# Performance work log

Measured on AMD Instinct MI355X. Metric: run time of the kernel, lower is better.

The kernel has to match this reference:

```python
import jax, jax.numpy as jnp
import numpy as np

NUM_ENT = 10000
NUM_REL = 230
S_DIM = 96
T_DIM = 32
DIM = S_DIM + T_DIM  # 128
N = 32768   # neighbors
Q = 4096    # unique query entities
E = 32768   # pooling edges
B = 1024    # batch triples
BN_EPS = 1e-5


def setup_inputs() -> dict:
    key = jax.random.key(0)
    ks = jax.random.split(key, 32)
    inp = {}
    inp["neighbor_idx"] = jax.random.randint(ks[0], (N,), 0, NUM_ENT)
    inp["rel_id"] = jax.random.randint(ks[1], (N,), 0, 2 * NUM_REL)
    inp["years"] = jax.random.uniform(ks[2], (N, 1), jnp.float32)
    inp["months"] = jax.random.uniform(ks[3], (N, 1), jnp.float32)
    inp["days"] = jax.random.uniform(ks[4], (N, 1), jnp.float32)
    inp["pool_src"] = jax.random.randint(ks[5], (E,), 0, N)
    inp["pool_dst"] = jax.random.randint(ks[6], (E,), 0, Q)
    inp["head_pos"] = jax.random.randint(ks[7], (B,), 0, Q)
    inp["tail_pos"] = jax.random.randint(ks[8], (B,), 0, Q)
    inp["rels"] = jax.random.randint(ks[9], (B,), 0, NUM_REL)
    # parameters (xavier-ish scales)
    inp["ent_embs"] = jax.random.normal(ks[10], (NUM_ENT, S_DIM), jnp.float32) * 0.05
    names = ["y_freq", "y_phi", "y_amp", "m_freq", "m_phi", "m_amp", "d_freq", "d_phi", "d_amp"]
    for i, n in enumerate(names):
        inp[n] = jax.random.normal(ks[11 + i], (NUM_ENT, T_DIM), jnp.float32) * 0.05
    inp["rel_embs"] = jax.random.normal(ks[20], (NUM_REL, DIM), jnp.float32) * 0.05
    inp["W"] = jax.random.normal(ks[21], (2 * NUM_REL, DIM, DIM), jnp.float32) * (1.0 / np.sqrt(DIM))
    inp["b"] = jnp.zeros((2 * NUM_REL, DIM), jnp.float32)
    inp["gamma"] = jnp.ones((2 * NUM_REL, DIM), jnp.float32)
    inp["beta"] = jnp.zeros((2 * NUM_REL, DIM), jnp.float32)
    return inp


def _forward(ent_embs, y_freq, y_phi, y_amp, m_freq, m_phi, m_amp,
             d_freq, d_phi, d_amp, rel_embs, W, b, gamma, beta,
             years, months, days,
             neighbor_idx, rel_id, pool_src, pool_dst, head_pos, tail_pos, rels):
    # diachronic time embedding: amp * sin(freq * t + phi), summed over y/m/d
    ty = y_amp[neighbor_idx] * jnp.sin(y_freq[neighbor_idx] * years + y_phi[neighbor_idx])
    tm = m_amp[neighbor_idx] * jnp.sin(m_freq[neighbor_idx] * months + m_phi[neighbor_idx])
    td = d_amp[neighbor_idx] * jnp.sin(d_freq[neighbor_idx] * days + d_phi[neighbor_idx])
    x = jnp.concatenate([ent_embs[neighbor_idx], ty + tm + td], axis=1)  # [N, DIM]

    # per-relation Linear (gather weights per neighbor)
    z = jnp.einsum('nd,nde->ne', x, W[rel_id]) + b[rel_id]  # [N, DIM]

    # per-relation-bucket BatchNorm (training stats, biased var); skipped for singleton buckets
    R2 = 2 * NUM_REL
    cnt = jax.ops.segment_sum(jnp.ones((z.shape[0],), z.dtype), rel_id, num_segments=R2)
    denom = jnp.maximum(cnt, 1.0)[:, None]
    mean = jax.ops.segment_sum(z, rel_id, num_segments=R2) / denom
    var = jax.ops.segment_sum(z * z, rel_id, num_segments=R2) / denom - mean * mean
    var = jnp.maximum(var, 0.0)
    zn = (z - mean[rel_id]) * jax.lax.rsqrt(var[rel_id] + BN_EPS) * gamma[rel_id] + beta[rel_id]
    z = jnp.where((cnt[rel_id] > 1.0)[:, None], zn, z)
    z = jax.nn.relu(z)

    # average pooling of neighbor features per query entity (PoolingLayer 'avg')
    psum = jax.ops.segment_sum(z[pool_src], pool_dst, num_segments=Q)
    pcnt = jax.ops.segment_sum(jnp.ones((pool_src.shape[0],), z.dtype), pool_dst, num_segments=Q)
    emb = psum / jnp.maximum(pcnt, 1.0)[:, None]  # [Q, DIM]

    # TransE-style scoring: -||h + r - t||_2 (dropout p=0 / eval mode)
    diff = emb[head_pos] + rel_embs[rels] - emb[tail_pos]
    return -jnp.sqrt(jnp.sum(diff * diff, axis=1))


def reference(neighbor_idx, rel_id, years, months, days, pool_src, pool_dst,
              head_pos, tail_pos, rels, ent_embs, y_freq, y_phi, y_amp,
              m_freq, m_phi, m_amp, d_freq, d_phi, d_amp, rel_embs, W, b, gamma, beta):
    return _forward(ent_embs, y_freq, y_phi, y_amp, m_freq, m_phi, m_amp,
                    d_freq, d_phi, d_amp, rel_embs, W, b, gamma, beta,
                    years, months, days,
                    neighbor_idx, rel_id, pool_src, pool_dst, head_pos, tail_pos, rels)
```

## Files before the change

kernel.cpp:

```cpp
#include <hip/hip_runtime.h>
#include <math.h>

#define NUM_ENT 10000
#define NUM_REL 230
#define R2      460
#define S_DIM   96
#define T_DIM   32
#define DIM     128
#define N_NBR   32768
#define Q_ENT   4096
#define E_EDGE  32768
#define B_TRI   1024
#define BN_EPS  1e-5f
#define CHUNK   64

typedef __attribute__((ext_vector_type(8))) short bf16x8;
typedef __attribute__((ext_vector_type(4))) float f32x4;

__device__ __forceinline__ unsigned short f2bf(float f) {
    unsigned int u = __float_as_uint(f);
    u = (u + 0x7FFFu + ((u >> 16) & 1u)) >> 16;
    return (unsigned short)u;
}

__device__ __forceinline__ int XIDX(int m, int d) {
    return (m * DIM + d) ^ ((m & 7) << 3);
}

__global__ void k_zero(int* __restrict__ p, int n4) {
    int i = blockIdx.x * blockDim.x + threadIdx.x;
    if (i < n4) ((int4*)p)[i] = make_int4(0, 0, 0, 0);
}

__global__ __launch_bounds__(256, 2) void k_front(
    const float* __restrict__ W, unsigned short* __restrict__ Wfrag,
    const int* __restrict__ rel, const int* __restrict__ pdst,
    int* __restrict__ hist_rel, int* __restrict__ hist_dst)
{
    const int t = threadIdx.x;
    if (blockIdx.x >= R2) {
        const int i = (blockIdx.x - R2) * 256 + t;
        if (i < N_NBR) atomicAdd(&hist_rel[rel[i]], 1);
        if (i < E_EDGE) atomicAdd(&hist_dst[pdst[i]], 1);
        return;
    }
    const int r = blockIdx.x;
    __shared__ float Wl[DIM * DIM];
    {
        const float4* Wg = (const float4*)(W + (size_t)r * DIM * DIM);
        float4* Wl4 = (float4*)Wl;
        #pragma unroll
        for (int i = 0; i < 16; ++i)
            Wl4[t + i * 256] = Wg[t + i * 256];
    }
    __syncthreads();
    unsigned short* dst = Wfrag + (size_t)r * DIM * DIM;
    #pragma unroll
    for (int it = 0; it < 8; ++it) {
        const int id = t + it * 256;
        const int lane = id & 63;
        const int h    = (id >> 6) & 1;
        const int wv   = (id >> 7) & 3;
        const int kk   = (id >> 9) & 3;
        const int n  = 32 * wv + 16 * h + (lane & 15);
        const int kb = 32 * kk + 8 * (lane >> 4);
        ushort4 lo, hi;
        lo.x = f2bf(Wl[(kb + 0) * DIM + n]);
        lo.y = f2bf(Wl[(kb + 1) * DIM + n]);
        lo.z = f2bf(Wl[(kb + 2) * DIM + n]);
        lo.w = f2bf(Wl[(kb + 3) * DIM + n]);
        hi.x = f2bf(Wl[(kb + 4) * DIM + n]);
        hi.y = f2bf(Wl[(kb + 5) * DIM + n]);
        hi.z = f2bf(Wl[(kb + 6) * DIM + n]);
        hi.w = f2bf(Wl[(kb + 7) * DIM + n]);
        *(ushort4*)&dst[id * 8]     = lo;
        *(ushort4*)&dst[id * 8 + 4] = hi;
    }
}

__global__ void k_scan_both(const int* __restrict__ hist_rel, int* __restrict__ offsets,
                            int* __restrict__ cur_rel,
                            const int* __restrict__ hist_dst, int* __restrict__ dst_off,
                            int* __restrict__ cur_dst)
{
    __shared__ int s[1024];
    const int t = threadIdx.x;
    if (blockIdx.x == 0) {
        const int h = (t < R2) ? hist_rel[t] : 0;
        if (t < 512) s[t] = h;
        __syncthreads();
        for (int off = 1; off < 512; off <<= 1) {
            int a = (t >= off && t < 512) ? s[t - off] : 0;
            __syncthreads();
            if (t < 512) s[t] += a;
            __syncthreads();
        }
        if (t == 0) offsets[0] = 0;
        if (t < R2) {
            offsets[t + 1] = s[t];
            cur_rel[t] = s[t] - h;
        }
    } else {
        const int base = t * 4;
        int v0 = hist_dst[base], v1 = hist_dst[base + 1];
        int v2 = hist_dst[base + 2], v3 = hist_dst[base + 3];
        s[t] = v0 + v1 + v2 + v3;
        __syncthreads();
        for (int off = 1; off < 1024; off <<= 1) {
            int a = (t >= off) ? s[t - off] : 0;
            __syncthreads();
            s[t] += a;
            __syncthreads();
        }
        int run = (t > 0) ? s[t - 1] : 0;
        dst_off[base] = run; cur_dst[base] = run; run += v0;
        dst_off[base + 1] = run; cur_dst[base + 1] = run; run += v1;
        dst_off[base + 2] = run; cur_dst[base + 2] = run; run += v2;
        dst_off[base + 3] = run; cur_dst[base + 3] = run; run += v3;
        if (t == 1023) dst_off[4096] = run;
    }
}

__global__ void k_scatter(const int* __restrict__ rel,
                          int* __restrict__ cur_rel, int* __restrict__ order,
                          int* __restrict__ rankpack,
                          const int* __restrict__ psrc, const int* __restrict__ pdst,
                          int* __restrict__ cur_dst, int* __restrict__ eorder_src) {
    int i = blockIdx.x * blockDim.x + threadIdx.x;
    if (i < N_NBR) {
        const int r = rel[i];
        const int pos = atomicAdd(&cur_rel[r], 1);
        order[pos] = i;
        rankpack[i] = pos | (r << 17);
    }
    if (i < E_EDGE) {
        eorder_src[atomicAdd(&cur_dst[pdst[i]], 1)] = psrc[i];
    }
}

__global__ __launch_bounds__(512, 4) void k_matvec(
    const int* __restrict__ order, const int* __restrict__ offsets,
    const int* __restrict__ nbr,
    const float* __restrict__ years, const float* __restrict__ months, const float* __restrict__ days,
    const float* __restrict__ ent,
    const float* __restrict__ yf, const float* __restrict__ yp, const float* __restrict__ ya,
    const float* __restrict__ mf, const float* __restrict__ mp, const float* __restrict__ ma,
    const float* __restrict__ df, const float* __restrict__ dp, const float* __restrict__ da,
    const unsigned short* __restrict__ Wfrag, const float* __restrict__ bias,
    const float* __restrict__ gamma, const float* __restrict__ beta,
    float* __restrict__ z_s, float* __restrict__ scale, float* __restrict__ shift)
{
    const int r     = blockIdx.x;
    const int start = offsets[r];
    const int cnt   = offsets[r + 1] - start;

    __shared__ __align__(16) unsigned short Xl[2][CHUNK * DIM];
    __shared__ int s_ord[2][CHUNK];
    __shared__ int s_ni[2][CHUNK];
    __shared__ float bnred[8][2][16][2];

    const int t    = threadIdx.x;
    const int wid  = t >> 6;
    const int half = wid >> 2;
    const int wv   = wid & 3;
    const int lane = t & 63;
    const int l15  = lane & 15;
    const int g    = lane >> 4;

    const int nn0 = 32 * wv + l15;
    const int nn1 = nn0 + 16;
    const float bv0 = bias[r * DIM + nn0];
    const float bv1 = bias[r * DIM + nn1];

    float lsum0 = 0.f, lsq0 = 0.f, lsum1 = 0.f, lsq1 = 0.f;
    const unsigned short* Wr = Wfrag + (size_t)r * DIM * DIM;

    for (int cbase = 0; cbase < cnt; cbase += 2 * CHUNK) {
        const int hbase = cbase + half * CHUNK;
        const int mcnt  = min(CHUNK, max(0, cnt - hbase));

        if (t < 2 * CHUNK) {
            const int hh = t >> 6;
            const int m  = t & 63;
            const int gb = cbase + hh * CHUNK;
            int o = -1, ni = 0;
            if (gb + m < cnt) { o = order[start + gb + m]; ni = nbr[o]; }
            s_ord[hh][m] = o;
            s_ni[hh][m]  = ni;
        }
        __syncthreads();

        if (mcnt > 0) {
            const int lt = t & 255;
            const int m = lt >> 2, s = lt & 3;
            const int ni = s_ni[half][m];
            const bool vm = (m < mcnt);
            #pragma unroll
            for (int kk = 0; kk < 6; ++kk) {
                const int d = 4 * (s + 4 * kk);
                float4 e = *(const float4*)(ent + (size_t)ni * S_DIM + d);
                ushort4 b;
                b.x = vm ? f2bf(e.x) : 0; b.y = vm ? f2bf(e.y) : 0;
                b.z = vm ? f2bf(e.z) : 0; b.w = vm ? f2bf(e.w) : 0;
                *(ushort4*)&Xl[half][XIDX(m, d)] = b;
            }
            const int o = s_ord[half][m] < 0 ? 0 : s_ord[half][m];
            const float yr = years[o], mo = months[o], dy = days[o];
            #pragma unroll
            for (int hh = 0; hh < 2; ++hh) {
                const int j0 = s * 8 + hh * 4;
                const size_t tb = (size_t)ni * T_DIM + j0;
                const float4 vyf = *(const float4*)(yf + tb), vyp = *(const float4*)(yp + tb), vya = *(const float4*)(ya + tb);
                const float4 vmf = *(const float4*)(mf + tb), vmp = *(const float4*)(mp + tb), vma = *(const float4*)(ma + tb);
                const float4 vdf = *(const float4*)(df + tb), vdp = *(const float4*)(dp + tb), vda = *(const float4*)(da + tb);
                ushort4 b;
                #pragma unroll
                for (int j = 0; j < 4; ++j) {
                    const float fy = ((const float*)&vyf)[j] * yr + ((const float*)&vyp)[j];
                    const float fm = ((const float*)&vmf)[j] * mo + ((const float*)&vmp)[j];
                    const float fd = ((const float*)&vdf)[j] * dy + ((const float*)&vdp)[j];
                    float v = ((const float*)&vya)[j] * sinf(fy)
                            + ((const float*)&vma)[j] * sinf(fm)
                            + ((const float*)&vda)[j] * sinf(fd);
                    ((unsigned short*)&b)[j] = vm ? f2bf(v) : 0;
                }
                *(ushort4*)&Xl[half][XIDX(m, S_DIM + j0)] = b;
            }
        }
        __syncthreads();

        if (mcnt > 0) {
            f32x4 acc[4][2];
            #pragma unroll
            for (int i = 0; i < 4; ++i)
                #pragma unroll
                for (int j = 0; j < 2; ++j) acc[i][j] = (f32x4)0.f;

            #pragma unroll
            for (int kk = 0; kk < 4; ++kk) {
                const int k0 = kk * 32;
                bf16x8 a[4];
                #pragma unroll
                for (int mt = 0; mt < 4; ++mt)
                    a[mt] = *(const bf16x8*)&Xl[half][XIDX(16 * mt + l15, k0 + 8 * g)];
                const bf16x8 b0 = *(const bf16x8*)&Wr[(size_t)((kk * 4 + wv) * 2 + 0) * 512 + lane * 8];
                const bf16x8 b1 = *(const bf16x8*)&Wr[(size_t)((kk * 4 + wv) * 2 + 1) * 512 + lane * 8];
                #pragma unroll
                for (int mt = 0; mt < 4; ++mt) {
                    acc[mt][0] = __builtin_amdgcn_mfma_f32_16x16x32_bf16(a[mt], b0, acc[mt][0], 0, 0, 0);
                    acc[mt][1] = __builtin_amdgcn_mfma_f32_16x16x32_bf16(a[mt], b1, acc[mt][1], 0, 0, 0);
                }
            }

            #pragma unroll
            for (int mt = 0; mt < 4; ++mt) {
                #pragma unroll
                for (int reg = 0; reg < 4; ++reg) {
                    const int ml = 16 * mt + 4 * g + reg;
                    if (ml < mcnt) {
                        const float v0 = acc[mt][0][reg] + bv0;
                        const float v1 = acc[mt][1][reg] + bv1;
                        const size_t row = (size_t)(start + hbase + ml) * DIM;
                        z_s[row + nn0] = v0;
                        z_s[row + nn1] = v1;
                        lsum0 += v0; lsq0 += v0 * v0;
                        lsum1 += v1; lsq1 += v1 * v1;
                    }
                }
            }
        }
        __syncthreads();
    }

    lsum0 += __shfl_xor(lsum0, 16); lsum0 += __shfl_xor(lsum0, 32);
    lsq0  += __shfl_xor(lsq0, 16);  lsq0  += __shfl_xor(lsq0, 32);
    lsum1 += __shfl_xor(lsum1, 16); lsum1 += __shfl_xor(lsum1, 32);
    lsq1  += __shfl_xor(lsq1, 16);  lsq1  += __shfl_xor(lsq1, 32);
    if (g == 0) {
        bnred[wid][0][l15][0] = lsum0; bnred[wid][0][l15][1] = lsq0;
        bnred[wid][1][l15][0] = lsum1; bnred[wid][1][l15][1] = lsq1;
    }
    __syncthreads();
    if (half == 0 && g == 0) {
        #pragma unroll
        for (int nt = 0; nt < 2; ++nt) {
            const int col = 32 * wv + 16 * nt + l15;
            const float s = bnred[wid][nt][l15][0] + bnred[wid + 4][nt][l15][0];
            const float q = bnred[wid][nt][l15][1] + bnred[wid + 4][nt][l15][1];
            float sc = 1.f, sh = 0.f;
            if (cnt > 1) {
                const float mean = s / (float)cnt;
                const float var  = fmaxf(q / (float)cnt - mean * mean, 0.f);
                const int gi = r * DIM + col;
                sc = gamma[gi] * rsqrtf(var + BN_EPS);
                sh = beta[gi] - mean * sc;
            }
            scale[r * DIM + col] = sc;
            shift[r * DIM + col] = sh;
        }
    }
}

__global__ void k_pool2(const int* __restrict__ eorder_src, const int* __restrict__ dst_off,
                        const int* __restrict__ rankpack,
                        const float* __restrict__ z_s,
                        const float* __restrict__ scale, const float* __restrict__ shift,
                        float* __restrict__ emb)
{
    const int q = blockIdx.x;
    const int d = threadIdx.x;
    const int e0 = dst_off[q], e1 = dst_off[q + 1];
    float acc = 0.f;
    for (int e = e0; e < e1; ++e) {
        const int pk = rankpack[eorder_src[e]];
        const int p  = pk & 0x1FFFF;
        const int r  = pk >> 17;
        const float v = z_s[(size_t)p * DIM + d] * scale[r * DIM + d] + shift[r * DIM + d];
        acc += fmaxf(v, 0.f);
    }
    emb[(size_t)q * DIM + d] = (e1 > e0) ? acc / (float)(e1 - e0) : 0.f;
}

__global__ void k_score(const int* __restrict__ head, const int* __restrict__ tail,
                        const int* __restrict__ rels,
                        const float* __restrict__ emb, const float* __restrict__ rel_embs,
                        float* __restrict__ out)
{
    const int b = blockIdx.x;
    const int d = threadIdx.x;
    const int h = head[b], tq = tail[b], r = rels[b];

    const float diff = emb[(size_t)h * DIM + d] + rel_embs[r * DIM + d]
                     - emb[(size_t)tq * DIM + d];
    float sq = diff * diff;
    for (int off = 32; off > 0; off >>= 1) sq += __shfl_down(sq, off);
    __shared__ float partial[2];
    if ((threadIdx.x & 63) == 0) partial[threadIdx.x >> 6] = sq;
    __syncthreads();
    if (threadIdx.x == 0) out[b] = -sqrtf(partial[0] + partial[1]);
}

extern "C" void kernel_launch(void* const* d_in, const int* in_sizes, int n_in,
                              void* d_out, int out_size, void* d_ws, size_t ws_size,
                              hipStream_t stream) {
    const int*   neighbor_idx = (const int*)  d_in[0];
    const int*   rel_id       = (const int*)  d_in[1];
    const float* years        = (const float*)d_in[2];
    const float* months       = (const float*)d_in[3];
    const float* days         = (const float*)d_in[4];
    const int*   pool_src     = (const int*)  d_in[5];
    const int*   pool_dst     = (const int*)  d_in[6];
    const int*   head_pos     = (const int*)  d_in[7];
    const int*   tail_pos     = (const int*)  d_in[8];
    const int*   rels         = (const int*)  d_in[9];
    const float* ent_embs     = (const float*)d_in[10];
    const float* y_freq       = (const float*)d_in[11];
    const float* y_phi        = (const float*)d_in[12];
    const float* y_amp        = (const float*)d_in[13];
    const float* m_freq       = (const float*)d_in[14];
    const float* m_phi        = (const float*)d_in[15];
    const float* m_amp        = (const float*)d_in[16];
    const float* d_freq       = (const float*)d_in[17];
    const float* d_phi        = (const float*)d_in[18];
    const float* d_amp        = (const float*)d_in[19];
    const float* rel_embs     = (const float*)d_in[20];
    const float* W            = (const float*)d_in[21];
    const float* bias         = (const float*)d_in[22];
    const float* gamma        = (const float*)d_in[23];
    const float* beta         = (const float*)d_in[24];

    float* out = (float*)d_out;

    float* ws = (float*)d_ws;
    size_t off = 0;
    unsigned short* Wfrag = (unsigned short*)(ws + off); off += (size_t)R2 * DIM * DIM / 2;
    float* z_s   = ws + off; off += (size_t)N_NBR * DIM;
    float* emb   = ws + off; off += (size_t)Q_ENT * DIM;
    float* scale = ws + off; off += (size_t)R2 * DIM;
    float* shift = ws + off; off += (size_t)R2 * DIM;
    int* hist_rel = (int*)(ws + off); off += R2;
    int* hist_dst = (int*)(ws + off); off += Q_ENT;
    int* offsets  = (int*)(ws + off); off += R2 + 1;
    int* cur_rel  = (int*)(ws + off); off += R2;
    int* dst_off  = (int*)(ws + off); off += Q_ENT + 1;
    int* cur_dst  = (int*)(ws + off); off += Q_ENT;
    int* order    = (int*)(ws + off); off += N_NBR;
    int* rankpack = (int*)(ws + off); off += N_NBR;
    int* eorder_src = (int*)(ws + off); off += E_EDGE;

    const int nzero4 = (R2 + Q_ENT + 3) / 4;
    k_zero<<<(nzero4 + 255) / 256, 256, 0, stream>>>(hist_rel, nzero4);

    k_front<<<R2 + (N_NBR + 255) / 256, 256, 0, stream>>>(
        W, Wfrag, rel_id, pool_dst, hist_rel, hist_dst);

    k_scan_both<<<2, 1024, 0, stream>>>(hist_rel, offsets, cur_rel,
                                        hist_dst, dst_off, cur_dst);

    k_scatter<<<(N_NBR + 255) / 256, 256, 0, stream>>>(rel_id, cur_rel, order, rankpack,
                                                       pool_src, pool_dst, cur_dst, eorder_src);

    k_matvec<<<R2, 512, 0, stream>>>(order, offsets, neighbor_idx,
                                     years, months, days, ent_embs,
                                     y_freq, y_phi, y_amp,
                                     m_freq, m_phi, m_amp,
                                     d_freq, d_phi, d_amp,
                                     Wfrag, bias, gamma, beta,
                                     z_s, scale, shift);

    k_pool2<<<Q_ENT, DIM, 0, stream>>>(eorder_src, dst_off, rankpack,
                                       z_s, scale, shift, emb);

    k_score<<<B_TRI, DIM, 0, stream>>>(head_pos, tail_pos, rels, emb, rel_embs, out);
}
```

Baseline: 76.75 us.

## Fuse W bf16 fragment conversion into matvec kernel via shared-memory staging

Result: no change. 77.26 us (+0.7%).

```diff
diff --git a/kernel.cpp b/kernel.cpp
--- a/kernel.cpp
+++ b/kernel.cpp
@@ -27,55 +27,20 @@
     return (m * DIM + d) ^ ((m & 7) << 3);
 }
 
+__device__ __forceinline__ int WSIDX(int k, int n) {
+    return k * DIM + (n ^ ((k & 7) << 2) ^ (((k >> 3) & 3) << 3));
+}
+
 __global__ void k_zero(int* __restrict__ p, int n4) {
     int i = blockIdx.x * blockDim.x + threadIdx.x;
     if (i < n4) ((int4*)p)[i] = make_int4(0, 0, 0, 0);
 }
 
-__global__ __launch_bounds__(256, 2) void k_front(
-    const float* __restrict__ W, unsigned short* __restrict__ Wfrag,
-    const int* __restrict__ rel, const int* __restrict__ pdst,
-    int* __restrict__ hist_rel, int* __restrict__ hist_dst)
-{
-    const int t = threadIdx.x;
-    if (blockIdx.x >= R2) {
-        const int i = (blockIdx.x - R2) * 256 + t;
-        if (i < N_NBR) atomicAdd(&hist_rel[rel[i]], 1);
-        if (i < E_EDGE) atomicAdd(&hist_dst[pdst[i]], 1);
-        return;
-    }
-    const int r = blockIdx.x;
-    __shared__ float Wl[DIM * DIM];
-    {
-        const float4* Wg = (const float4*)(W + (size_t)r * DIM * DIM);
-        float4* Wl4 = (float4*)Wl;
-        #pragma unroll
-        for (int i = 0; i < 16; ++i)
-            Wl4[t + i * 256] = Wg[t + i * 256];
-    }
-    __syncthreads();
-    unsigned short* dst = Wfrag + (size_t)r * DIM * DIM;
-    #pragma unroll
-    for (int it = 0; it < 8; ++it) {
-        const int id = t + it * 256;
-        const int lane = id & 63;
-        const int h    = (id >> 6) & 1;
-        const int wv   = (id >> 7) & 3;
-        const int kk   = (id >> 9) & 3;
-        const int n  = 32 * wv + 16 * h + (lane & 15);
-        const int kb = 32 * kk + 8 * (lane >> 4);
-        ushort4 lo, hi;
-        lo.x = f2bf(Wl[(kb + 0) * DIM + n]);
-        lo.y = f2bf(Wl[(kb + 1) * DIM + n]);
-        lo.z = f2bf(Wl[(kb + 2) * DIM + n]);
-        lo.w = f2bf(Wl[(kb + 3) * DIM + n]);
-        hi.x = f2bf(Wl[(kb + 4) * DIM + n]);
-        hi.y = f2bf(Wl[(kb + 5) * DIM + n]);
-        hi.z = f2bf(Wl[(kb + 6) * DIM + n]);
-        hi.w = f2bf(Wl[(kb + 7) * DIM + n]);
-        *(ushort4*)&dst[id * 8]     = lo;
-        *(ushort4*)&dst[id * 8 + 4] = hi;
-    }
+__global__ void k_hist(const int* __restrict__ rel, const int* __restrict__ pdst,
+                       int* __restrict__ hist_rel, int* __restrict__ hist_dst) {
+    int i = blockIdx.x * blockDim.x + threadIdx.x;
+    if (i < N_NBR) atomicAdd(&hist_rel[rel[i]], 1);
+    if (i < E_EDGE) atomicAdd(&hist_dst[pdst[i]], 1);
 }
 
 __global__ void k_scan_both(const int* __restrict__ hist_rel, int* __restrict__ offsets,
@@ -146,7 +111,7 @@
     const float* __restrict__ yf, const float* __restrict__ yp, const float* __restrict__ ya,
     const float* __restrict__ mf, const float* __restrict__ mp, const float* __restrict__ ma,
     const float* __restrict__ df, const float* __restrict__ dp, const float* __restrict__ da,
-    const unsigned short* __restrict__ Wfrag, const float* __restrict__ bias,
+    const float* __restrict__ W, const float* __restrict__ bias,
     const float* __restrict__ gamma, const float* __restrict__ beta,
     float* __restrict__ z_s, float* __restrict__ scale, float* __restrict__ shift)
 {
@@ -154,6 +119,7 @@
     const int start = offsets[r];
     const int cnt   = offsets[r + 1] - start;
 
+    __shared__ __align__(16) unsigned short Wl[DIM * DIM];
     __shared__ __align__(16) unsigned short Xl[2][CHUNK * DIM];
     __shared__ int s_ord[2][CHUNK];
     __shared__ int s_ni[2][CHUNK];
@@ -167,13 +133,52 @@
     const int l15  = lane & 15;
     const int g    = lane >> 4;
 
+    {
+        float* Xf = (float*)&Xl[0][0];
+        #pragma unroll
+        for (int p = 0; p < 2; ++p) {
+            const float4* Wg = (const float4*)(W + (size_t)r * DIM * DIM + p * 8192);
+            #pragma unroll
+            for (int i = 0; i < 4; ++i) {
+                const int c  = t + i * 512;
+                const int k  = c >> 5;
+                const int n4 = (c & 31) * 4;
+                *(float4*)&Xf[WSIDX(k, n4)] = Wg[c];
+            }
+            __syncthreads();
+            #pragma unroll
+            for (int i = 0; i < 2; ++i) {
+                const int id  = t + i * 512;
+                const int sid = p * 1024 + id;
+                const int sl  = sid & 63;
+                const int sh_ = (sid >> 6) & 1;
+                const int swv = (sid >> 7) & 3;
+                const int skk = (sid >> 9) & 3;
+                const int n   = 32 * swv + 16 * sh_ + (sl & 15);
+                const int kbl = 32 * skk + 8 * (sl >> 4) - 64 * p;
+                const int sg  = sl >> 4;
+                ushort4 lo, hi;
+                lo.x = f2bf(Xf[(kbl + 0) * DIM + (n ^ 0  ^ (sg << 3))]);
+                lo.y = f2bf(Xf[(kbl + 1) * DIM + (n ^ 4  ^ (sg << 3))]);
+                lo.z = f2bf(Xf[(kbl + 2) * DIM + (n ^ 8  ^ (sg << 3))]);
+                lo.w = f2bf(Xf[(kbl + 3) * DIM + (n ^ 12 ^ (sg << 3))]);
+                hi.x = f2bf(Xf[(kbl + 4) * DIM + (n ^ 16 ^ (sg << 3))]);
+                hi.y = f2bf(Xf[(kbl + 5) * DIM + (n ^ 20 ^ (sg << 3))]);
+                hi.z = f2bf(Xf[(kbl + 6) * DIM + (n ^ 24 ^ (sg << 3))]);
+                hi.w = f2bf(Xf[(kbl + 7) * DIM + (n ^ 28 ^ (sg << 3))]);
+                *(ushort4*)&Wl[sid * 8]     = lo;
+                *(ushort4*)&Wl[sid * 8 + 4] = hi;
+            }
+            __syncthreads();
+        }
+    }
+
     const int nn0 = 32 * wv + l15;
     const int nn1 = nn0 + 16;
     const float bv0 = bias[r * DIM + nn0];
     const float bv1 = bias[r * DIM + nn1];
 
     float lsum0 = 0.f, lsq0 = 0.f, lsum1 = 0.f, lsq1 = 0.f;
-    const unsigned short* Wr = Wfrag + (size_t)r * DIM * DIM;
 
     for (int cbase = 0; cbase < cnt; cbase += 2 * CHUNK) {
         const int hbase = cbase + half * CHUNK;
@@ -243,8 +248,8 @@
                 #pragma unroll
                 for (int mt = 0; mt < 4; ++mt)
                     a[mt] = *(const bf16x8*)&Xl[half][XIDX(16 * mt + l15, k0 + 8 * g)];
-                const bf16x8 b0 = *(const bf16x8*)&Wr[(size_t)((kk * 4 + wv) * 2 + 0) * 512 + lane * 8];
-                const bf16x8 b1 = *(const bf16x8*)&Wr[(size_t)((kk * 4 + wv) * 2 + 1) * 512 + lane * 8];
+                const bf16x8 b0 = *(const bf16x8*)&Wl[((kk * 4 + wv) * 2 + 0) * 512 + lane * 8];
+                const bf16x8 b1 = *(const bf16x8*)&Wl[((kk * 4 + wv) * 2 + 1) * 512 + lane * 8];
                 #pragma unroll
                 for (int mt = 0; mt < 4; ++mt) {
                     acc[mt][0] = __builtin_amdgcn_mfma_f32_16x16x32_bf16(a[mt], b0, acc[mt][0], 0, 0, 0);
@@ -373,7 +378,6 @@
 
     float* ws = (float*)d_ws;
     size_t off = 0;
-    unsigned short* Wfrag = (unsigned short*)(ws + off); off += (size_t)R2 * DIM * DIM / 2;
     float* z_s   = ws + off; off += (size_t)N_NBR * DIM;
     float* emb   = ws + off; off += (size_t)Q_ENT * DIM;
     float* scale = ws + off; off += (size_t)R2 * DIM;
@@ -391,8 +395,7 @@
     const int nzero4 = (R2 + Q_ENT + 3) / 4;
     k_zero<<<(nzero4 + 255) / 256, 256, 0, stream>>>(hist_rel, nzero4);
 
-    k_front<<<R2 + (N_NBR + 255) / 256, 256, 0, stream>>>(
-        W, Wfrag, rel_id, pool_dst, hist_rel, hist_dst);
+    k_hist<<<(N_NBR + 255) / 256, 256, 0, stream>>>(rel_id, pool_dst, hist_rel, hist_dst);
 
     k_scan_both<<<2, 1024, 0, stream>>>(hist_rel, offsets, cur_rel,
                                         hist_dst, dst_off, cur_dst);
@@ -405,7 +408,7 @@
                                      y_freq, y_phi, y_amp,
                                      m_freq, m_phi, m_amp,
                                      d_freq, d_phi, d_amp,
-                                     Wfrag, bias, gamma, beta,
+                                     W, bias, gamma, beta,
                                      z_s, scale, shift);
 
     k_pool2<<<Q_ENT, DIM, 0, stream>>>(eorder_src, dst_off, rankpack,
```
